# Kernel optimization log

Measured on AMD Instinct MI355X. Metric: run time of the kernel, lower is better.

Reference implementation:

```python
import jax, jax.numpy as jnp
import numpy as np

DIM_IN, DIM_H, DIM_OUT = 1024, 512, 256
E, T, B = 8, 4, 16384


def setup_inputs() -> dict:
    key = jax.random.key(0)
    ks = jax.random.split(key, 8)
    s1 = 1.0 / np.sqrt(DIM_IN)
    s2 = 1.0 / np.sqrt(DIM_H)
    x = jax.random.normal(ks[0], (B, DIM_IN), dtype=jnp.float32)
    # stacked expert params: layer1 [E, H, IN], layer2 [E, OUT, H]
    W1 = jax.random.uniform(ks[1], (E, DIM_H, DIM_IN), jnp.float32, -s1, s1)
    b1 = jax.random.uniform(ks[2], (E, DIM_H), jnp.float32, -s1, s1)
    W2 = jax.random.uniform(ks[3], (E, DIM_OUT, DIM_H), jnp.float32, -s2, s2)
    b2 = jax.random.uniform(ks[4], (E, DIM_OUT), jnp.float32, -s2, s2)
    # gate params: [T, E, IN]
    Wg = jax.random.uniform(ks[5], (T, E, DIM_IN), jnp.float32, -s1, s1)
    bg = jax.random.uniform(ks[6], (T, E), jnp.float32, -s1, s1)
    return {"x": x, "W1": W1, "b1": b1, "W2": W2, "b2": b2, "Wg": Wg, "bg": bg}


def reference(x, W1, b1, W2, b2, Wg, bg):
    # Experts: Linear+ReLU, Linear+ReLU (dropout=0 / eval mode)
    h = jax.nn.relu(jnp.einsum('bi,ehi->beh', x, W1) + b1)          # [B,E,H]
    feats = jax.nn.relu(jnp.einsum('beh,edh->bed', h, W2) + b2)     # [B,E,D]
    # Gates: softmax over experts, one gate per task
    logits = jnp.einsum('bi,tei->bte', x, Wg) + bg                  # [B,T,E]
    w = jax.nn.softmax(logits, axis=-1)                             # [B,T,E]
    # Weighted combine: einsum('bde,be->bd') per task
    out = jnp.einsum('bed,bte->tbd', feats, w)                      # [T,B,D]
    return out
```

## Files before the change

### kernel.cpp

```cpp
#include <hip/hip_runtime.h>


typedef __attribute__((ext_vector_type(8))) __bf16 bf16x8;
typedef __attribute__((ext_vector_type(4))) float f32x4;
typedef __attribute__((ext_vector_type(8))) unsigned short u16x8;

__device__ __forceinline__ float bf2f(unsigned short u) {
  union { unsigned int i; float f; } x;
  x.i = ((unsigned int)u) << 16;
  return x.f;
}

__device__ __forceinline__ unsigned short f2bf(float f) {
  union { float f; unsigned int i; } x;
  x.f = f;
  unsigned int r = x.i + 0x7FFFu + ((x.i >> 16) & 1u);
  return (unsigned short)(r >> 16);
}

__device__ __forceinline__ void gload_lds16(const unsigned short* g, unsigned short* l) {
  __builtin_amdgcn_global_load_lds(
      (const __attribute__((address_space(1))) void*)g,
      (__attribute__((address_space(3))) void*)l, 16, 0, 0);
}

__global__ void cvt_k(const float* __restrict__ in, unsigned short* __restrict__ out, int n4) {
  int i = blockIdx.x * blockDim.x + threadIdx.x;
  if (i >= n4) return;
  float4 v = ((const float4*)in)[i];
  ushort4 o;
  o.x = f2bf(v.x); o.y = f2bf(v.y); o.z = f2bf(v.z); o.w = f2bf(v.w);
  ((ushort4*)out)[i] = o;
}

__global__ __launch_bounds__(256) void gates_k(
    const unsigned short* __restrict__ xb,
    const unsigned short* __restrict__ Wgb,
    const float* __restrict__ bg,
    float* __restrict__ gw)
{
  const int lane = threadIdx.x & 63;
  const int wid = threadIdx.x >> 6;
  const int wgid = blockIdx.x * 4 + wid;
  const int brow = wgid * 16;
  const int l15 = lane & 15, lhi = lane >> 4;

  f32x4 acc0 = {0.f, 0.f, 0.f, 0.f};
  f32x4 acc1 = {0.f, 0.f, 0.f, 0.f};
  for (int k0 = 0; k0 < 1024; k0 += 32) {
    bf16x8 a  = *(const bf16x8*)&xb[(size_t)(brow + l15) * 1024 + k0 + lhi * 8];
    bf16x8 b0 = *(const bf16x8*)&Wgb[(size_t)l15 * 1024 + k0 + lhi * 8];
    bf16x8 b1 = *(const bf16x8*)&Wgb[(size_t)(16 + l15) * 1024 + k0 + lhi * 8];
    acc0 = __builtin_amdgcn_mfma_f32_16x16x32_bf16(a, b0, acc0, 0, 0, 0);
    acc1 = __builtin_amdgcn_mfma_f32_16x16x32_bf16(a, b1, acc1, 0, 0, 0);
  }
  const float bg0 = bg[l15];
  const float bg1 = bg[16 + l15];
#pragma unroll
  for (int r = 0; r < 4; ++r) {
    float v0 = acc0[r] + bg0;
    float v1 = acc1[r] + bg1;
    float m0 = v0, m1 = v1;
#pragma unroll
    for (int d = 1; d <= 4; d <<= 1) {
      m0 = fmaxf(m0, __shfl_xor(m0, d));
      m1 = fmaxf(m1, __shfl_xor(m1, d));
    }
    float e0 = __expf(v0 - m0), e1 = __expf(v1 - m1);
    float s0 = e0, s1 = e1;
#pragma unroll
    for (int d = 1; d <= 4; d <<= 1) {
      s0 += __shfl_xor(s0, d);
      s1 += __shfl_xor(s1, d);
    }
    int b = brow + lhi * 4 + r;
    gw[(size_t)b * 32 + l15]      = e0 / s0;
    gw[(size_t)b * 32 + 16 + l15] = e1 / s1;
  }
}

template <bool RELU>
__global__ __launch_bounds__(512, 2) void gemm256(
    const unsigned short* __restrict__ A, int lda, int aZ,
    const unsigned short* __restrict__ B,
    const float* __restrict__ bias,
    unsigned short* __restrict__ C, int ldc, int cZ,
    int tilesN, int N, int K)
{
  extern __shared__ char smem_raw[];
  unsigned short* lds = (unsigned short*)smem_raw;
  char* ldsb = (char*)smem_raw;

  const int tid = threadIdx.x;
  const int lane = tid & 63, wid = tid >> 6;
  const int wr = wid >> 2, wc = wid & 3;
  const int l15 = lane & 15, lhi = lane >> 4;

  const int nwg = gridDim.x;
  const int cpx = nwg >> 3;
  const int wg = blockIdx.x;
  const int swz = (wg & 7) * cpx + (wg >> 3);
  const int rt = swz / tilesN, ct = swz - rt * tilesN;
  const int brow = rt * 256, bcol = ct * 256;
  const int e = blockIdx.z;

  const unsigned short* Ab = A + (size_t)e * aZ + (size_t)brow * lda;
  const unsigned short* Bb = B + (size_t)e * N * K + (size_t)bcol * K;
  const float* biasb = bias + (size_t)e * N;
  unsigned short* Cb = C + (size_t)e * cZ;

  const int NT = K >> 6;
  const int NI = NT >> 1;

  const int trow = tid >> 3;
  const int cg8 = (((tid & 7) ^ (trow & 7)) << 3);

  const int axor = (l15 & 7) << 4;
  const int koff0 = (lhi << 4) ^ axor;
  const int koff1 = (64 + (lhi << 4)) ^ axor;

  const char* pA0 = ldsb + wr * 16384 + l15 * 128 + koff0;
  const char* pA1 = ldsb + wr * 16384 + l15 * 128 + koff1;
  const char* pB0 = ldsb + 65536 + wc * 8192 + l15 * 128 + koff0;
  const char* pB1 = ldsb + 65536 + wc * 8192 + l15 * 128 + koff1;

  f32x4 bias4[4];
#pragma unroll
  for (int nf = 0; nf < 4; ++nf)
    bias4[nf] = *(const f32x4*)&biasb[bcol + wc * 64 + nf * 16 + lhi * 4];

  const f32x4 zero = {0.f, 0.f, 0.f, 0.f};
  f32x4 acc[8][4];
#pragma unroll
  for (int m = 0; m < 8; ++m)
#pragma unroll
    for (int n = 0; n < 4; ++n) acc[m][n] = zero;

  auto STAGE_A = [&](int slot, int t, int u) {
    gload_lds16(Ab + (size_t)(u * 64 + trow) * lda + (t * 64 + cg8),
                lds + slot * 16384 + u * 4096 + wid * 512);
  };
  auto STAGE_B = [&](int slot, int t, int u) {
    gload_lds16(Bb + (size_t)(u * 64 + trow) * K + (t * 64 + cg8),
                lds + 32768 + slot * 16384 + u * 4096 + wid * 512);
  };

#pragma unroll
  for (int u = 0; u < 4; ++u) STAGE_B(0, 0, u);
#pragma unroll
  for (int u = 0; u < 4; ++u) STAGE_A(0, 0, u);
  asm volatile("s_waitcnt vmcnt(0)" ::: "memory");
  __builtin_amdgcn_s_barrier();

  auto ktile = [&](int slot, int tn, bool stageNext) {
    bf16x8 af[4][2], bfr[4][2];
#pragma unroll
    for (int mi = 0; mi < 4; ++mi) {
      af[mi][0] = *(const bf16x8*)(pA0 + slot * 32768 + mi * 2048);
      af[mi][1] = *(const bf16x8*)(pA1 + slot * 32768 + mi * 2048);
    }
#pragma unroll
    for (int n = 0; n < 2; ++n) {
      bfr[n][0] = *(const bf16x8*)(pB0 + slot * 32768 + n * 2048);
      bfr[n][1] = *(const bf16x8*)(pB1 + slot * 32768 + n * 2048);
    }
    if (stageNext) { STAGE_B(slot ^ 1, tn, 0); STAGE_B(slot ^ 1, tn, 1); }
    __builtin_amdgcn_s_barrier();
    __builtin_amdgcn_s_setprio(1);
#pragma unroll
    for (int kk = 0; kk < 2; ++kk)
#pragma unroll
      for (int mi = 0; mi < 4; ++mi)
#pragma unroll
        for (int n = 0; n < 2; ++n)
          acc[mi][n] = __builtin_amdgcn_mfma_f32_16x16x32_bf16(bfr[n][kk], af[mi][kk], acc[mi][n], 0, 0, 0);
    __builtin_amdgcn_s_setprio(0);
    __builtin_amdgcn_s_barrier();

#pragma unroll
    for (int n = 0; n < 2; ++n) {
      bfr[2 + n][0] = *(const bf16x8*)(pB0 + slot * 32768 + (2 + n) * 2048);
      bfr[2 + n][1] = *(const bf16x8*)(pB1 + slot * 32768 + (2 + n) * 2048);
    }
    if (stageNext) { STAGE_B(slot ^ 1, tn, 2); STAGE_B(slot ^ 1, tn, 3); }
    __builtin_amdgcn_s_barrier();
    __builtin_amdgcn_s_setprio(1);
#pragma unroll
    for (int kk = 0; kk < 2; ++kk)
#pragma unroll
      for (int mi = 0; mi < 4; ++mi)
#pragma unroll
        for (int n = 0; n < 2; ++n)
          acc[mi][2 + n] = __builtin_amdgcn_mfma_f32_16x16x32_bf16(bfr[2 + n][kk], af[mi][kk], acc[mi][2 + n], 0, 0, 0);
    __builtin_amdgcn_s_setprio(0);
    asm volatile("s_waitcnt vmcnt(4)" ::: "memory");
    __builtin_amdgcn_s_barrier();

#pragma unroll
    for (int mi = 0; mi < 4; ++mi) {
      af[mi][0] = *(const bf16x8*)(pA0 + slot * 32768 + 8192 + mi * 2048);
      af[mi][1] = *(const bf16x8*)(pA1 + slot * 32768 + 8192 + mi * 2048);
    }
    if (stageNext) { STAGE_A(slot ^ 1, tn, 0); STAGE_A(slot ^ 1, tn, 2); }
    __builtin_amdgcn_s_barrier();
    __builtin_amdgcn_s_setprio(1);
#pragma unroll
    for (int kk = 0; kk < 2; ++kk)
#pragma unroll
      for (int mi = 0; mi < 4; ++mi)
#pragma unroll
        for (int n = 0; n < 2; ++n)
          acc[4 + mi][n] = __builtin_amdgcn_mfma_f32_16x16x32_bf16(bfr[n][kk], af[mi][kk], acc[4 + mi][n], 0, 0, 0);
    __builtin_amdgcn_s_setprio(0);
    __builtin_amdgcn_s_barrier();

    if (stageNext) { STAGE_A(slot ^ 1, tn, 1); STAGE_A(slot ^ 1, tn, 3); }
    __builtin_amdgcn_s_barrier();
    __builtin_amdgcn_s_setprio(1);
#pragma unroll
    for (int kk = 0; kk < 2; ++kk)
#pragma unroll
      for (int mi = 0; mi < 4; ++mi)
#pragma unroll
        for (int n = 0; n < 2; ++n)
          acc[4 + mi][2 + n] = __builtin_amdgcn_mfma_f32_16x16x32_bf16(bfr[2 + n][kk], af[mi][kk], acc[4 + mi][2 + n], 0, 0, 0);
    __builtin_amdgcn_s_setprio(0);
    asm volatile("s_waitcnt vmcnt(2)" ::: "memory");
    __builtin_amdgcn_s_barrier();
  };

#pragma unroll 1
  for (int i = 0; i < NI; ++i) {
    ktile(0, 2 * i + 1, true);
    ktile(1, 2 * i + 2, (2 * i + 2) < NT);
  }

#pragma unroll
  for (int mf = 0; mf < 8; ++mf) {
    const size_t rowoff = (size_t)(brow + wr * 128 + mf * 16 + l15) * ldc;
#pragma unroll
    for (int nf = 0; nf < 4; ++nf) {
      const int col = bcol + wc * 64 + nf * 16 + lhi * 4;
      f32x4 v = acc[mf][nf];
      ushort4 o;
      float v0 = v[0] + bias4[nf][0];
      float v1 = v[1] + bias4[nf][1];
      float v2 = v[2] + bias4[nf][2];
      float v3 = v[3] + bias4[nf][3];
      if (RELU) {
        v0 = v0 > 0.f ? v0 : 0.f;
        v1 = v1 > 0.f ? v1 : 0.f;
        v2 = v2 > 0.f ? v2 : 0.f;
        v3 = v3 > 0.f ? v3 : 0.f;
      }
      o.x = f2bf(v0); o.y = f2bf(v1); o.z = f2bf(v2); o.w = f2bf(v3);
      *(ushort4*)&Cb[rowoff + col] = o;
    }
  }
}

template <bool RELU>
__global__ __launch_bounds__(256) void gemm_bt(
    const unsigned short* __restrict__ A, int lda, int aZ,
    const unsigned short* __restrict__ B,
    const float* __restrict__ bias,
    unsigned short* __restrict__ C, int ldc, int cZ,
    int N, int K)
{
  __shared__ unsigned short As[128 * 64];
  __shared__ unsigned short Bs[128 * 64];
  const int tid = threadIdx.x;
  const int wid = tid >> 6;
  const int lane = tid & 63;
  const int wr = wid >> 1, wc = wid & 1;
  const int l15 = lane & 15, lhi = lane >> 4;
  const int b = blockIdx.x;
  const int brow = (((b >> 4) << 3) + (b & 7)) * 128;
  const int bcol = ((b >> 3) & 1) * 128;
  const int e = blockIdx.z;

  const unsigned short* Ab = A + (size_t)e * aZ;
  const unsigned short* Bb = B + (size_t)e * N * K;
  const float* biasb = bias + (size_t)e * N;
  unsigned short* Cb = C + (size_t)e * cZ;

  const f32x4 zero = {0.f, 0.f, 0.f, 0.f};
  f32x4 acc[4][4];
#pragma unroll
  for (int m = 0; m < 4; ++m)
#pragma unroll
    for (int n = 0; n < 4; ++n) acc[m][n] = zero;

  const int srow = lane >> 3;
  const int scol = (lane & 7) * 8;
  const int rbase = wid * 32;

  for (int k0 = 0; k0 < K; k0 += 64) {
#pragma unroll
    for (int i = 0; i < 4; ++i) {
      int r = rbase + i * 8;
      gload_lds16(Ab + (size_t)(brow + r + srow) * lda + (k0 + scol), &As[r * 64]);
    }
#pragma unroll
    for (int i = 0; i < 4; ++i) {
      int r = rbase + i * 8;
      gload_lds16(Bb + (size_t)(bcol + r + srow) * K + (k0 + scol), &Bs[r * 64]);
    }
    __syncthreads();
#pragma unroll
    for (int kk = 0; kk < 2; ++kk) {
      bf16x8 af[4], bfr[4];
#pragma unroll
      for (int m = 0; m < 4; ++m)
        af[m] = *(const bf16x8*)&As[(wr * 64 + m * 16 + l15) * 64 + kk * 32 + lhi * 8];
#pragma unroll
      for (int n = 0; n < 4; ++n)
        bfr[n] = *(const bf16x8*)&Bs[(wc * 64 + n * 16 + l15) * 64 + kk * 32 + lhi * 8];
#pragma unroll
      for (int m = 0; m < 4; ++m)
#pragma unroll
        for (int n = 0; n < 4; ++n)
          acc[m][n] = __builtin_amdgcn_mfma_f32_16x16x32_bf16(af[m], bfr[n], acc[m][n], 0, 0, 0);
    }
    __syncthreads();
  }

#pragma unroll
  for (int n = 0; n < 4; ++n) {
    int col = bcol + wc * 64 + n * 16 + l15;
    float bv = biasb[col];
#pragma unroll
    for (int m = 0; m < 4; ++m) {
      int row0 = brow + wr * 64 + m * 16 + lhi * 4;
#pragma unroll
      for (int r = 0; r < 4; ++r) {
        float v = acc[m][n][r] + bv;
        if (RELU) v = v > 0.f ? v : 0.f;
        Cb[(size_t)(row0 + r) * ldc + col] = f2bf(v);
      }
    }
  }
}

__global__ __launch_bounds__(256) void combine_k(
    const unsigned short* __restrict__ feats,
    const float* __restrict__ gw,
    float* __restrict__ out)
{
  int tid = blockIdx.x * 256 + threadIdx.x;
  int b = tid >> 5;
  int d0 = (tid & 31) * 8;

  const f32x4* wv4 = (const f32x4*)(gw + (size_t)b * 32);
  f32x4 wv[8];
#pragma unroll
  for (int i = 0; i < 8; ++i) wv[i] = wv4[i];

  float o[4][8];
#pragma unroll
  for (int t = 0; t < 4; ++t)
#pragma unroll
    for (int j = 0; j < 8; ++j) o[t][j] = 0.f;

#pragma unroll
  for (int e = 0; e < 8; ++e) {
    u16x8 fv = *(const u16x8*)&feats[((size_t)b * 8 + e) * 256 + d0];
    float f[8];
#pragma unroll
    for (int j = 0; j < 8; ++j) f[j] = bf2f(fv[j]);
#pragma unroll
    for (int t = 0; t < 4; ++t) {
      float wt = wv[(t * 8 + e) >> 2][(t * 8 + e) & 3];
#pragma unroll
      for (int j = 0; j < 8; ++j) o[t][j] += wt * f[j];
    }
  }
#pragma unroll
  for (int t = 0; t < 4; ++t) {
    f32x4* dst = (f32x4*)(out + ((size_t)t * 16384 + b) * 256 + d0);
    f32x4 s0 = {o[t][0], o[t][1], o[t][2], o[t][3]};
    f32x4 s1 = {o[t][4], o[t][5], o[t][6], o[t][7]};
    dst[0] = s0;
    dst[1] = s1;
  }
}

extern "C" void kernel_launch(void* const* d_in, const int* in_sizes, int n_in,
                              void* d_out, int out_size, void* d_ws, size_t ws_size,
                              hipStream_t stream) {
  (void)in_sizes; (void)n_in; (void)out_size; (void)ws_size;
  const float* x  = (const float*)d_in[0];
  const float* W1 = (const float*)d_in[1];
  const float* b1 = (const float*)d_in[2];
  const float* W2 = (const float*)d_in[3];
  const float* b2 = (const float*)d_in[4];
  const float* Wg = (const float*)d_in[5];
  const float* bg = (const float*)d_in[6];
  float* out = (float*)d_out;

  char* ws = (char*)d_ws;
  unsigned short* xb    = (unsigned short*)ws; ws += (size_t)16384 * 1024 * 2;
  unsigned short* W1b   = (unsigned short*)ws; ws += (size_t)4096 * 1024 * 2;
  unsigned short* W2b   = (unsigned short*)ws; ws += (size_t)2048 * 512 * 2;
  unsigned short* Wgb   = (unsigned short*)ws; ws += (size_t)32 * 1024 * 2;
  float*          gw    = (float*)ws;         ws += (size_t)16384 * 32 * 4;
  unsigned short* H     = (unsigned short*)ws; ws += (size_t)16384 * 4096 * 2;
  unsigned short* feats = (unsigned short*)ws; ws += (size_t)16384 * 2048 * 2;

  cvt_k<<<16384, 256, 0, stream>>>(x, xb, 16384 * 1024 / 4);
  cvt_k<<<4096, 256, 0, stream>>>(W1, W1b, 4096 * 1024 / 4);
  cvt_k<<<1024, 256, 0, stream>>>(W2, W2b, 2048 * 512 / 4);
  cvt_k<<<32, 256, 0, stream>>>(Wg, Wgb, 32 * 1024 / 4);

  gates_k<<<256, 256, 0, stream>>>(xb, Wgb, bg, gw);

  gemm256<true><<<dim3(1024, 1, 1), 512, 131072, stream>>>(
      xb, 1024, 0, W1b, b1, H, 4096, 0, 16, 4096, 1024);

  gemm_bt<true><<<dim3(256, 1, 8), 256, 0, stream>>>(
      H, 4096, 512, W2b, b2, feats, 2048, 256, 256, 512);

  combine_k<<<2048, 256, 0, stream>>>(feats, gw, out);
}
```

Measured before the change: 287.2 us.

## Switch big GEMM to 32x32x16 MFMA and fuse x conversion into gates kernel

The main layer-1 GEMM now issues 32x32x16 bf16 MFMAs instead of 16x16x32, with LDS fragment addressing, bias loads and the epilogue rebuilt for the 32x32 accumulator layout. Each wave does fewer, larger MFMAs and fewer LDS fragment reads per tile. Separately, the fp32-to-bf16 conversion of x moves into the gates kernel, which converts its 64-row slice before computing gate logits, removing one launch. The trade-off is that the gates kernel now does the conversion with only 256 blocks, so that step may use the GPU less fully.

```diff
diff --git a/kernel.cpp b/kernel.cpp
--- a/kernel.cpp
+++ b/kernel.cpp
@@ -3,6 +3,7 @@
 
 typedef __attribute__((ext_vector_type(8))) __bf16 bf16x8;
 typedef __attribute__((ext_vector_type(4))) float f32x4;
+typedef __attribute__((ext_vector_type(16))) float f32x16;
 typedef __attribute__((ext_vector_type(8))) unsigned short u16x8;
 
 __device__ __forceinline__ float bf2f(unsigned short u) {
@@ -34,15 +35,28 @@
 }
 
 __global__ __launch_bounds__(256) void gates_k(
-    const unsigned short* __restrict__ xb,
+    const float* __restrict__ x,
+    unsigned short* __restrict__ xb,
     const unsigned short* __restrict__ Wgb,
     const float* __restrict__ bg,
     float* __restrict__ gw)
 {
+  const int rowbase = blockIdx.x * 64;
+  {
+    const float4* xsrc = (const float4*)(x + (size_t)rowbase * 1024);
+    ushort4* xdst = (ushort4*)(xb + (size_t)rowbase * 1024);
+    for (int i = threadIdx.x; i < 64 * 256; i += 256) {
+      float4 v = xsrc[i];
+      ushort4 o;
+      o.x = f2bf(v.x); o.y = f2bf(v.y); o.z = f2bf(v.z); o.w = f2bf(v.w);
+      xdst[i] = o;
+    }
+  }
+  __syncthreads();
+
   const int lane = threadIdx.x & 63;
   const int wid = threadIdx.x >> 6;
-  const int wgid = blockIdx.x * 4 + wid;
-  const int brow = wgid * 16;
+  const int brow = rowbase + wid * 16;
   const int l15 = lane & 15, lhi = lane >> 4;
 
   f32x4 acc0 = {0.f, 0.f, 0.f, 0.f};
@@ -94,7 +108,7 @@
   const int tid = threadIdx.x;
   const int lane = tid & 63, wid = tid >> 6;
   const int wr = wid >> 2, wc = wid & 3;
-  const int l15 = lane & 15, lhi = lane >> 4;
+  const int l31 = lane & 31, hi = lane >> 5;
 
   const int nwg = gridDim.x;
   const int cpx = nwg >> 3;
@@ -115,26 +129,28 @@
   const int trow = tid >> 3;
   const int cg8 = (((tid & 7) ^ (trow & 7)) << 3);
 
-  const int axor = (l15 & 7) << 4;
-  const int koff0 = (lhi << 4) ^ axor;
-  const int koff1 = (64 + (lhi << 4)) ^ axor;
-
-  const char* pA0 = ldsb + wr * 16384 + l15 * 128 + koff0;
-  const char* pA1 = ldsb + wr * 16384 + l15 * 128 + koff1;
-  const char* pB0 = ldsb + 65536 + wc * 8192 + l15 * 128 + koff0;
-  const char* pB1 = ldsb + 65536 + wc * 8192 + l15 * 128 + koff1;
-
-  f32x4 bias4[4];
-#pragma unroll
-  for (int nf = 0; nf < 4; ++nf)
-    bias4[nf] = *(const f32x4*)&biasb[bcol + wc * 64 + nf * 16 + lhi * 4];
-
-  const f32x4 zero = {0.f, 0.f, 0.f, 0.f};
-  f32x4 acc[8][4];
-#pragma unroll
-  for (int m = 0; m < 8; ++m)
-#pragma unroll
-    for (int n = 0; n < 4; ++n) acc[m][n] = zero;
+  const int axor = (lane & 7) << 4;
+  int koff[4];
+#pragma unroll
+  for (int ks = 0; ks < 4; ++ks) koff[ks] = ((ks << 5) | (hi << 4)) ^ axor;
+
+  const char* pA = ldsb + wr * 16384 + l31 * 128;
+  const char* pB = ldsb + 65536 + wc * 8192 + l31 * 128;
+
+  f32x4 bias4[2][4];
+#pragma unroll
+  for (int ni = 0; ni < 2; ++ni)
+#pragma unroll
+    for (int rq = 0; rq < 4; ++rq)
+      bias4[ni][rq] = *(const f32x4*)&biasb[bcol + wc * 64 + ni * 32 + rq * 8 + hi * 4];
+
+  f32x16 acc[4][2];
+#pragma unroll
+  for (int m = 0; m < 4; ++m)
+#pragma unroll
+    for (int n = 0; n < 2; ++n)
+#pragma unroll
+      for (int r = 0; r < 16; ++r) acc[m][n][r] = 0.f;
 
   auto STAGE_A = [&](int slot, int t, int u) {
     gload_lds16(Ab + (size_t)(u * 64 + trow) * lda + (t * 64 + cg8),
@@ -153,64 +169,54 @@
   __builtin_amdgcn_s_barrier();
 
   auto ktile = [&](int slot, int tn, bool stageNext) {
-    bf16x8 af[4][2], bfr[4][2];
-#pragma unroll
-    for (int mi = 0; mi < 4; ++mi) {
-      af[mi][0] = *(const bf16x8*)(pA0 + slot * 32768 + mi * 2048);
-      af[mi][1] = *(const bf16x8*)(pA1 + slot * 32768 + mi * 2048);
-    }
-#pragma unroll
-    for (int n = 0; n < 2; ++n) {
-      bfr[n][0] = *(const bf16x8*)(pB0 + slot * 32768 + n * 2048);
-      bfr[n][1] = *(const bf16x8*)(pB1 + slot * 32768 + n * 2048);
-    }
+    bf16x8 af[2][4], bf[2][4];
+#pragma unroll
+    for (int mi = 0; mi < 2; ++mi)
+#pragma unroll
+      for (int ks = 0; ks < 4; ++ks)
+        af[mi][ks] = *(const bf16x8*)(pA + slot * 32768 + mi * 4096 + koff[ks]);
+#pragma unroll
+    for (int ks = 0; ks < 4; ++ks)
+      bf[0][ks] = *(const bf16x8*)(pB + slot * 32768 + koff[ks]);
     if (stageNext) { STAGE_B(slot ^ 1, tn, 0); STAGE_B(slot ^ 1, tn, 1); }
     __builtin_amdgcn_s_barrier();
     __builtin_amdgcn_s_setprio(1);
 #pragma unroll
-    for (int kk = 0; kk < 2; ++kk)
-#pragma unroll
-      for (int mi = 0; mi < 4; ++mi)
-#pragma unroll
-        for (int n = 0; n < 2; ++n)
-          acc[mi][n] = __builtin_amdgcn_mfma_f32_16x16x32_bf16(bfr[n][kk], af[mi][kk], acc[mi][n], 0, 0, 0);
+    for (int ks = 0; ks < 4; ++ks)
+#pragma unroll
+      for (int mi = 0; mi < 2; ++mi)
+        acc[mi][0] = __builtin_amdgcn_mfma_f32_32x32x16_bf16(bf[0][ks], af[mi][ks], acc[mi][0], 0, 0, 0);
     __builtin_amdgcn_s_setprio(0);
     __builtin_amdgcn_s_barrier();
 
 #pragma unroll
-    for (int n = 0; n < 2; ++n) {
-      bfr[2 + n][0] = *(const bf16x8*)(pB0 + slot * 32768 + (2 + n) * 2048);
-      bfr[2 + n][1] = *(const bf16x8*)(pB1 + slot * 32768 + (2 + n) * 2048);
-    }
+    for (int ks = 0; ks < 4; ++ks)
+      bf[1][ks] = *(const bf16x8*)(pB + slot * 32768 + 4096 + koff[ks]);
     if (stageNext) { STAGE_B(slot ^ 1, tn, 2); STAGE_B(slot ^ 1, tn, 3); }
     __builtin_amdgcn_s_barrier();
     __builtin_amdgcn_s_setprio(1);
 #pragma unroll
-    for (int kk = 0; kk < 2; ++kk)
-#pragma unroll
-      for (int mi = 0; mi < 4; ++mi)
-#pragma unroll
-        for (int n = 0; n < 2; ++n)
-          acc[mi][2 + n] = __builtin_amdgcn_mfma_f32_16x16x32_bf16(bfr[2 + n][kk], af[mi][kk], acc[mi][2 + n], 0, 0, 0);
+    for (int ks = 0; ks < 4; ++ks)
+#pragma unroll
+      for (int mi = 0; mi < 2; ++mi)
+        acc[mi][1] = __builtin_amdgcn_mfma_f32_32x32x16_bf16(bf[1][ks], af[mi][ks], acc[mi][1], 0, 0, 0);
     __builtin_amdgcn_s_setprio(0);
     asm volatile("s_waitcnt vmcnt(4)" ::: "memory");
     __builtin_amdgcn_s_barrier();
 
 #pragma unroll
-    for (int mi = 0; mi < 4; ++mi) {
-      af[mi][0] = *(const bf16x8*)(pA0 + slot * 32768 + 8192 + mi * 2048);
-      af[mi][1] = *(const bf16x8*)(pA1 + slot * 32768 + 8192 + mi * 2048);
-    }
+    for (int mi = 0; mi < 2; ++mi)
+#pragma unroll
+      for (int ks = 0; ks < 4; ++ks)
+        af[mi][ks] = *(const bf16x8*)(pA + slot * 32768 + (2 + mi) * 4096 + koff[ks]);
     if (stageNext) { STAGE_A(slot ^ 1, tn, 0); STAGE_A(slot ^ 1, tn, 2); }
     __builtin_amdgcn_s_barrier();
     __builtin_amdgcn_s_setprio(1);
 #pragma unroll
-    for (int kk = 0; kk < 2; ++kk)
-#pragma unroll
-      for (int mi = 0; mi < 4; ++mi)
-#pragma unroll
-        for (int n = 0; n < 2; ++n)
-          acc[4 + mi][n] = __builtin_amdgcn_mfma_f32_16x16x32_bf16(bfr[n][kk], af[mi][kk], acc[4 + mi][n], 0, 0, 0);
+    for (int ks = 0; ks < 4; ++ks)
+#pragma unroll
+      for (int mi = 0; mi < 2; ++mi)
+        acc[2 + mi][0] = __builtin_amdgcn_mfma_f32_32x32x16_bf16(bf[0][ks], af[mi][ks], acc[2 + mi][0], 0, 0, 0);
     __builtin_amdgcn_s_setprio(0);
     __builtin_amdgcn_s_barrier();
 
@@ -218,12 +224,10 @@
     __builtin_amdgcn_s_barrier();
     __builtin_amdgcn_s_setprio(1);
 #pragma unroll
-    for (int kk = 0; kk < 2; ++kk)
-#pragma unroll
-      for (int mi = 0; mi < 4; ++mi)
-#pragma unroll
-        for (int n = 0; n < 2; ++n)
-          acc[4 + mi][2 + n] = __builtin_amdgcn_mfma_f32_16x16x32_bf16(bfr[2 + n][kk], af[mi][kk], acc[4 + mi][2 + n], 0, 0, 0);
+    for (int ks = 0; ks < 4; ++ks)
+#pragma unroll
+      for (int mi = 0; mi < 2; ++mi)
+        acc[2 + mi][1] = __builtin_amdgcn_mfma_f32_32x32x16_bf16(bf[1][ks], af[mi][ks], acc[2 + mi][1], 0, 0, 0);
     __builtin_amdgcn_s_setprio(0);
     asm volatile("s_waitcnt vmcnt(2)" ::: "memory");
     __builtin_amdgcn_s_barrier();
@@ -236,25 +240,27 @@
   }
 
 #pragma unroll
-  for (int mf = 0; mf < 8; ++mf) {
-    const size_t rowoff = (size_t)(brow + wr * 128 + mf * 16 + l15) * ldc;
-#pragma unroll
-    for (int nf = 0; nf < 4; ++nf) {
-      const int col = bcol + wc * 64 + nf * 16 + lhi * 4;
-      f32x4 v = acc[mf][nf];
-      ushort4 o;
-      float v0 = v[0] + bias4[nf][0];
-      float v1 = v[1] + bias4[nf][1];
-      float v2 = v[2] + bias4[nf][2];
-      float v3 = v[3] + bias4[nf][3];
-      if (RELU) {
-        v0 = v0 > 0.f ? v0 : 0.f;
-        v1 = v1 > 0.f ? v1 : 0.f;
-        v2 = v2 > 0.f ? v2 : 0.f;
-        v3 = v3 > 0.f ? v3 : 0.f;
+  for (int mi = 0; mi < 4; ++mi) {
+    const size_t rowoff = (size_t)(brow + wr * 128 + mi * 32 + l31) * ldc;
+#pragma unroll
+    for (int ni = 0; ni < 2; ++ni) {
+#pragma unroll
+      for (int rq = 0; rq < 4; ++rq) {
+        const int col = bcol + wc * 64 + ni * 32 + rq * 8 + hi * 4;
+        float v0 = acc[mi][ni][rq * 4 + 0] + bias4[ni][rq][0];
+        float v1 = acc[mi][ni][rq * 4 + 1] + bias4[ni][rq][1];
+        float v2 = acc[mi][ni][rq * 4 + 2] + bias4[ni][rq][2];
+        float v3 = acc[mi][ni][rq * 4 + 3] + bias4[ni][rq][3];
+        if (RELU) {
+          v0 = v0 > 0.f ? v0 : 0.f;
+          v1 = v1 > 0.f ? v1 : 0.f;
+          v2 = v2 > 0.f ? v2 : 0.f;
+          v3 = v3 > 0.f ? v3 : 0.f;
+        }
+        ushort4 o;
+        o.x = f2bf(v0); o.y = f2bf(v1); o.z = f2bf(v2); o.w = f2bf(v3);
+        *(ushort4*)&Cb[rowoff + col] = o;
       }
-      o.x = f2bf(v0); o.y = f2bf(v1); o.z = f2bf(v2); o.w = f2bf(v3);
-      *(ushort4*)&Cb[rowoff + col] = o;
     }
   }
 }
@@ -407,12 +413,11 @@
   unsigned short* H     = (unsigned short*)ws; ws += (size_t)16384 * 4096 * 2;
   unsigned short* feats = (unsigned short*)ws; ws += (size_t)16384 * 2048 * 2;
 
-  cvt_k<<<16384, 256, 0, stream>>>(x, xb, 16384 * 1024 / 4);
   cvt_k<<<4096, 256, 0, stream>>>(W1, W1b, 4096 * 1024 / 4);
   cvt_k<<<1024, 256, 0, stream>>>(W2, W2b, 2048 * 512 / 4);
   cvt_k<<<32, 256, 0, stream>>>(Wg, Wgb, 32 * 1024 / 4);
 
-  gates_k<<<256, 256, 0, stream>>>(xb, Wgb, bg, gw);
+  gates_k<<<256, 256, 0, stream>>>(x, xb, Wgb, bg, gw);
 
   gemm256<true><<<dim3(1024, 1, 1), 512, 131072, stream>>>(
       xb, 1024, 0, W1b, b1, H, 4096, 0, 16, 4096, 1024);
```

After: 336.4 us. +17.1%, slower.
